# Kernel optimization log

Measured on AMD Instinct MI355X. Metric: run time of the kernel, lower is better.

Reference implementation:

```python
import jax, jax.numpy as jnp
import numpy as np

N_BINS = 15


def setup_inputs() -> dict:
    key = jax.random.key(0)
    k1, k2 = jax.random.split(key)
    N, C = 262144, 1000
    logits = jax.random.normal(k1, (N, C), dtype=jnp.float32)
    labels = jax.random.randint(k2, (N,), 0, C, dtype=jnp.int64)
    return {"logits": logits, "labels": labels}


def reference(logits, labels):
    # softmax + max over classes -> per-sample confidence and prediction
    probs = jax.nn.softmax(logits, axis=1)
    confidences = jnp.max(probs, axis=1)            # [N]
    predictions = jnp.argmax(probs, axis=1)         # [N]
    accuracies = (predictions == labels).astype(confidences.dtype)

    # Bin b covers (b/n_bins, (b+1)/n_bins]  (lower exclusive, upper inclusive),
    # matching conf > lower & conf <= upper: bin = ceil(conf*n_bins) - 1.
    bin_idx = jnp.clip(
        jnp.ceil(confidences * N_BINS).astype(jnp.int32) - 1, 0, N_BINS - 1
    )

    n = confidences.shape[0]
    counts = jax.ops.segment_sum(jnp.ones_like(confidences), bin_idx, num_segments=N_BINS)
    conf_sum = jax.ops.segment_sum(confidences, bin_idx, num_segments=N_BINS)
    acc_sum = jax.ops.segment_sum(accuracies, bin_idx, num_segments=N_BINS)

    safe = jnp.maximum(counts, 1.0)
    avg_conf = conf_sum / safe
    avg_acc = acc_sum / safe
    prop = counts / n
    ece = jnp.sum(jnp.where(counts > 0, jnp.abs(avg_conf - avg_acc) * prop, 0.0))
    return ece
```

## Files before the change

### kernel.cpp

```cpp
#include <hip/hip_runtime.h>
#include <math.h>

#define NBINS 15

__global__ void ece_zero_ws(float* ws) {
    int i = threadIdx.x;
    if (i < NBINS * 3) ws[i] = 0.0f;
}

__global__ void __launch_bounds__(256, 8) ece_main(
    const float* __restrict__ logits, const int* __restrict__ labels,
    float* __restrict__ ws, int N, int C) {
    __shared__ float lds[NBINS * 3];
    if (threadIdx.x < NBINS * 3) lds[threadIdx.x] = 0.0f;
    __syncthreads();

    const int lane = threadIdx.x & 63;
    const int wid  = blockIdx.x * (blockDim.x >> 6) + (threadIdx.x >> 6);
    const int nw   = gridDim.x * (blockDim.x >> 6);
    const int nvec = C >> 2;
    const int tail = nvec << 2;

    for (int row = wid; row < N; row += nw) {
        const float4* rp = (const float4*)(logits + (size_t)row * (size_t)C);
        float m = -INFINITY;
        float s = 0.0f;
        int   mi = 0x7fffffff;

        for (int i = lane; i < nvec; i += 64) {
            float4 x = rp[i];
            int gi = i << 2;
            {   float v = x.x;
                if (v > m) { s = s * __expf(m - v) + 1.0f; m = v; mi = gi; }
                else       { s += __expf(v - m); } }
            {   float v = x.y;
                if (v > m) { s = s * __expf(m - v) + 1.0f; m = v; mi = gi + 1; }
                else       { s += __expf(v - m); } }
            {   float v = x.z;
                if (v > m) { s = s * __expf(m - v) + 1.0f; m = v; mi = gi + 2; }
                else       { s += __expf(v - m); } }
            {   float v = x.w;
                if (v > m) { s = s * __expf(m - v) + 1.0f; m = v; mi = gi + 3; }
                else       { s += __expf(v - m); } }
        }
        for (int i = tail + lane; i < C; i += 64) {
            float v = logits[(size_t)row * (size_t)C + i];
            if (v > m) { s = s * __expf(m - v) + 1.0f; m = v; mi = i; }
            else       { s += __expf(v - m); }
        }

        #pragma unroll
        for (int off = 32; off >= 1; off >>= 1) {
            float om  = __shfl_xor(m, off);
            float os  = __shfl_xor(s, off);
            int   omi = __shfl_xor(mi, off);
            float nm  = fmaxf(m, om);
            float e1  = (m  > -INFINITY) ? __expf(m  - nm) : 0.0f;
            float e2  = (om > -INFINITY) ? __expf(om - nm) : 0.0f;
            s = s * e1 + os * e2;
            if (om > m || (om == m && omi < mi)) mi = omi;
            m = nm;
        }

        if (lane == 0) {
            float conf = 1.0f / s;
            float acc  = (labels[row] == mi) ? 1.0f : 0.0f;
            int b = (int)ceilf(conf * (float)NBINS) - 1;
            b = b < 0 ? 0 : (b > NBINS - 1 ? NBINS - 1 : b);
            atomicAdd(&lds[b * 3 + 0], 1.0f);
            atomicAdd(&lds[b * 3 + 1], conf);
            atomicAdd(&lds[b * 3 + 2], acc);
        }
    }

    __syncthreads();
    if (threadIdx.x < NBINS * 3) atomicAdd(&ws[threadIdx.x], lds[threadIdx.x]);
}

__global__ void ece_final(const float* __restrict__ ws, float* __restrict__ out, float n) {
    if (threadIdx.x == 0) {
        float ece = 0.0f;
        #pragma unroll
        for (int b = 0; b < NBINS; ++b) {
            float c  = ws[b * 3 + 0];
            float cs = ws[b * 3 + 1];
            float as = ws[b * 3 + 2];
            if (c > 0.0f) ece += fabsf(cs / c - as / c) * (c / n);
        }
        out[0] = ece;
    }
}

extern "C" void kernel_launch(void* const* d_in, const int* in_sizes, int n_in,
                              void* d_out, int out_size, void* d_ws, size_t ws_size,
                              hipStream_t stream) {
    const float* logits = (const float*)d_in[0];
    const int*   labels = (const int*)d_in[1];
    float* out = (float*)d_out;
    float* ws  = (float*)d_ws;

    const int N = in_sizes[1];
    const int C = in_sizes[0] / in_sizes[1];

    ece_zero_ws<<<1, 64, 0, stream>>>(ws);

    const int threads = 256;
    int waves_needed = N;
    int blocks = (waves_needed + (threads / 64) - 1) / (threads / 64);
    if (blocks > 2048) blocks = 2048;
    ece_main<<<blocks, threads, 0, stream>>>(logits, labels, ws, N, C);

    ece_final<<<1, 64, 0, stream>>>(ws, out, (float)N);
}
```

Measured before the change: 209.3 us.

## Hold each softmax row in registers and use a two-pass max/sum

For C divisible by 4 and at most 2048, each wave loads the whole row into registers with nontemporal vector loads. It then computes the max with a wave reduction and sums the exponentials against that global max, which removes the branchy online-softmax rescaling and the exp-heavy combine shuffles. Launch bounds drop from 8 to 4 blocks per CU to make room for the extra registers, at some cost in occupancy and memory-latency hiding. A generic scalar fallback handles other shapes.

```diff
diff --git a/kernel.cpp b/kernel.cpp
--- a/kernel.cpp
+++ b/kernel.cpp
@@ -1,14 +1,18 @@
 #include <hip/hip_runtime.h>
 #include <math.h>
+#include <limits.h>
 
 #define NBINS 15
+
+typedef float f32x4 __attribute__((ext_vector_type(4)));
 
 __global__ void ece_zero_ws(float* ws) {
     int i = threadIdx.x;
     if (i < NBINS * 3) ws[i] = 0.0f;
 }
 
-__global__ void __launch_bounds__(256, 8) ece_main(
+template <int NV>
+__global__ void __launch_bounds__(256, 4) ece_main_reg(
     const float* __restrict__ logits, const int* __restrict__ labels,
     float* __restrict__ ws, int N, int C) {
     __shared__ float lds[NBINS * 3];
@@ -19,36 +23,87 @@
     const int wid  = blockIdx.x * (blockDim.x >> 6) + (threadIdx.x >> 6);
     const int nw   = gridDim.x * (blockDim.x >> 6);
     const int nvec = C >> 2;
-    const int tail = nvec << 2;
 
     for (int row = wid; row < N; row += nw) {
-        const float4* rp = (const float4*)(logits + (size_t)row * (size_t)C);
+        const f32x4* rp = (const f32x4*)(logits + (size_t)row * (size_t)C);
+
+        f32x4 r[NV];
+        #pragma unroll
+        for (int j = 0; j < NV; ++j) {
+            int idx = lane + j * 64;
+            if (idx < nvec) {
+                r[j] = __builtin_nontemporal_load(&rp[idx]);
+            } else {
+                r[j] = (f32x4){-INFINITY, -INFINITY, -INFINITY, -INFINITY};
+            }
+        }
+
+        float m = -INFINITY;
+        #pragma unroll
+        for (int j = 0; j < NV; ++j) {
+            m = fmaxf(m, fmaxf(fmaxf(r[j].x, r[j].y), fmaxf(r[j].z, r[j].w)));
+        }
+        #pragma unroll
+        for (int off = 32; off >= 1; off >>= 1)
+            m = fmaxf(m, __shfl_xor(m, off));
+
+        float s = 0.0f;
+        int   mi = INT_MAX;
+        #pragma unroll
+        for (int j = 0; j < NV; ++j) {
+            int gi = (lane + j * 64) << 2;
+            float ex = __expf(r[j].x - m);
+            float ey = __expf(r[j].y - m);
+            float ez = __expf(r[j].z - m);
+            float ew = __expf(r[j].w - m);
+            s += (ex + ey) + (ez + ew);
+            if (r[j].x == m) mi = min(mi, gi);
+            if (r[j].y == m) mi = min(mi, gi + 1);
+            if (r[j].z == m) mi = min(mi, gi + 2);
+            if (r[j].w == m) mi = min(mi, gi + 3);
+        }
+        #pragma unroll
+        for (int off = 32; off >= 1; off >>= 1) {
+            s += __shfl_xor(s, off);
+            mi = min(mi, __shfl_xor(mi, off));
+        }
+
+        if (lane == 0) {
+            float conf = 1.0f / s;
+            float acc  = (labels[row] == mi) ? 1.0f : 0.0f;
+            int b = (int)ceilf(conf * (float)NBINS) - 1;
+            b = b < 0 ? 0 : (b > NBINS - 1 ? NBINS - 1 : b);
+            atomicAdd(&lds[b * 3 + 0], 1.0f);
+            atomicAdd(&lds[b * 3 + 1], conf);
+            atomicAdd(&lds[b * 3 + 2], acc);
+        }
+    }
+
+    __syncthreads();
+    if (threadIdx.x < NBINS * 3) atomicAdd(&ws[threadIdx.x], lds[threadIdx.x]);
+}
+
+__global__ void __launch_bounds__(256, 4) ece_main_gen(
+    const float* __restrict__ logits, const int* __restrict__ labels,
+    float* __restrict__ ws, int N, int C) {
+    __shared__ float lds[NBINS * 3];
+    if (threadIdx.x < NBINS * 3) lds[threadIdx.x] = 0.0f;
+    __syncthreads();
+
+    const int lane = threadIdx.x & 63;
+    const int wid  = blockIdx.x * (blockDim.x >> 6) + (threadIdx.x >> 6);
+    const int nw   = gridDim.x * (blockDim.x >> 6);
+
+    for (int row = wid; row < N; row += nw) {
+        const float* rp = logits + (size_t)row * (size_t)C;
         float m = -INFINITY;
         float s = 0.0f;
-        int   mi = 0x7fffffff;
-
-        for (int i = lane; i < nvec; i += 64) {
-            float4 x = rp[i];
-            int gi = i << 2;
-            {   float v = x.x;
-                if (v > m) { s = s * __expf(m - v) + 1.0f; m = v; mi = gi; }
-                else       { s += __expf(v - m); } }
-            {   float v = x.y;
-                if (v > m) { s = s * __expf(m - v) + 1.0f; m = v; mi = gi + 1; }
-                else       { s += __expf(v - m); } }
-            {   float v = x.z;
-                if (v > m) { s = s * __expf(m - v) + 1.0f; m = v; mi = gi + 2; }
-                else       { s += __expf(v - m); } }
-            {   float v = x.w;
-                if (v > m) { s = s * __expf(m - v) + 1.0f; m = v; mi = gi + 3; }
-                else       { s += __expf(v - m); } }
-        }
-        for (int i = tail + lane; i < C; i += 64) {
-            float v = logits[(size_t)row * (size_t)C + i];
+        int   mi = INT_MAX;
+        for (int i = lane; i < C; i += 64) {
+            float v = rp[i];
             if (v > m) { s = s * __expf(m - v) + 1.0f; m = v; mi = i; }
             else       { s += __expf(v - m); }
         }
-
         #pragma unroll
         for (int off = 32; off >= 1; off >>= 1) {
             float om  = __shfl_xor(m, off);
@@ -61,7 +116,6 @@
             if (om > m || (om == m && omi < mi)) mi = omi;
             m = nm;
         }
-
         if (lane == 0) {
             float conf = 1.0f / s;
             float acc  = (labels[row] == mi) ? 1.0f : 0.0f;
@@ -105,10 +159,16 @@
     ece_zero_ws<<<1, 64, 0, stream>>>(ws);
 
     const int threads = 256;
-    int waves_needed = N;
-    int blocks = (waves_needed + (threads / 64) - 1) / (threads / 64);
+    int blocks = (N + (threads / 64) - 1) / (threads / 64);
     if (blocks > 2048) blocks = 2048;
-    ece_main<<<blocks, threads, 0, stream>>>(logits, labels, ws, N, C);
+
+    if ((C & 3) == 0 && C <= 4 * 64 * 4) {
+        ece_main_reg<4><<<blocks, threads, 0, stream>>>(logits, labels, ws, N, C);
+    } else if ((C & 3) == 0 && C <= 8 * 64 * 4) {
+        ece_main_reg<8><<<blocks, threads, 0, stream>>>(logits, labels, ws, N, C);
+    } else {
+        ece_main_gen<<<blocks, threads, 0, stream>>>(logits, labels, ws, N, C);
+    }
 
     ece_final<<<1, 64, 0, stream>>>(ws, out, (float)N);
 }
```

Result: faster. 185.3 us (-11.5%).
